# Kernel optimization log

Hardware: AMD Instinct MI355X
Metric: run time of the kernel (lower is better)

The kernel has to match this reference:

```python
import jax, jax.numpy as jnp
import numpy as np

N = 200_000      # total nodes
E = 3_200_000    # directed edges
F = 128          # input features
G = 2_000        # graphs in batch
SIZES = (128, 128, 128, 128, 128, 64)
K = 2            # TAGConv hops
EPS = 1e-5


def setup_inputs() -> dict:
    key = jax.random.key(0)
    ks = jax.random.split(key, 12)
    x = jax.random.normal(ks[0], (N, F), jnp.float32)
    edge_index = jax.random.randint(ks[1], (2, E), 0, N, dtype=jnp.int32).astype(jnp.int64)
    segment_ids = jnp.sort(jax.random.randint(ks[2], (N,), 0, G, dtype=jnp.int32)).astype(jnp.int64)
    conv_W = jax.random.normal(ks[3], (5, (K + 1) * 128, 128), jnp.float32) * 0.05
    conv_W_last = jax.random.normal(ks[4], ((K + 1) * 128, 64), jnp.float32) * 0.05
    bn_gamma = jnp.ones((5, 128), jnp.float32)
    bn_beta = jnp.zeros((5, 128), jnp.float32)
    bn_gamma_last = jnp.ones((64,), jnp.float32)
    bn_beta_last = jnp.zeros((64,), jnp.float32)
    agg_bn_gamma = jnp.ones((4,), jnp.float32)
    agg_bn_beta = jnp.zeros((4,), jnp.float32)
    agg_W = jax.random.normal(ks[5], (64, 4 * 64), jnp.float32) * 0.05
    agg_b = jnp.zeros((64,), jnp.float32)
    out_W = jax.random.normal(ks[6], (1, 64), jnp.float32) * 0.05
    out_b = jnp.zeros((1,), jnp.float32)
    return dict(x=x, edge_index=edge_index, segment_ids=segment_ids, conv_W=conv_W,
                conv_W_last=conv_W_last, bn_gamma=bn_gamma, bn_beta=bn_beta,
                bn_gamma_last=bn_gamma_last, bn_beta_last=bn_beta_last,
                agg_bn_gamma=agg_bn_gamma, agg_bn_beta=agg_bn_beta,
                agg_W=agg_W, agg_b=agg_b, out_W=out_W, out_b=out_b)


def _forward(x, edge_index, segment_ids, conv_W, conv_W_last, bn_gamma, bn_beta,
             bn_gamma_last, bn_beta_last, agg_bn_gamma, agg_bn_beta,
             agg_W, agg_b, out_W, out_b):
    src, dst = edge_index[0], edge_index[1]
    deg = jax.ops.segment_sum(jnp.ones((E,), x.dtype), dst, num_segments=N)
    norm = jnp.where(deg > 0, jax.lax.rsqrt(jnp.maximum(deg, 1.0)), 0.0)[:, None]  # D^{-1/2}

    def prop(h):  # h: [N, d] -> D^{-1/2} A D^{-1/2} h
        return norm * jax.ops.segment_sum((h * norm)[src], dst, num_segments=N)

    def tagconv(h, W):  # concat of A_norm^k h for k=0..K, then linear (no bias; BN follows)
        hs = [h]
        for _ in range(K):
            hs.append(prop(hs[-1]))
        return jnp.concatenate(hs, axis=-1) @ W

    def bn(h, g, b):  # training-mode batchnorm over nodes
        m = h.mean(0)
        v = h.var(0)
        return (h - m) * jax.lax.rsqrt(v + EPS) * g + b

    outs = []
    h = x
    for l in range(len(SIZES)):
        if l < 5:
            W, g, b = conv_W[l], bn_gamma[l], bn_beta[l]
        else:
            W, g, b = conv_W_last, bn_gamma_last, bn_beta_last
        h = jax.nn.relu(bn(tagconv(h, W), g, b))
        if l >= 2 and SIZES[l] == SIZES[l - 2]:  # skip connection
            h = h + outs[l - 2]
        outs.append(h)

    # ragged pooling: (max, min, mean, std) per graph
    counts = jax.ops.segment_sum(jnp.ones((N,), h.dtype), segment_ids, num_segments=G)[:, None]
    s = jax.ops.segment_sum(h, segment_ids, num_segments=G)
    mean = s / jnp.maximum(counts, 1.0)
    ssq = jax.ops.segment_sum(h * h, segment_ids, num_segments=G)
    var = (ssq - counts * mean * mean) / jnp.maximum(counts - 1.0, 1.0)  # unbiased like th.std
    std = jnp.sqrt(jnp.maximum(var, 0.0))
    mx = jax.ops.segment_max(h, segment_ids, num_segments=G)
    mn = jax.ops.segment_min(h, segment_ids, num_segments=G)
    pooled = jnp.stack([mx, mn, mean, std], axis=1)  # [G, 4, 64]

    # aggregation BatchNorm1d over the 4 pooling channels (stats over graphs x feat)
    m = pooled.mean(axis=(0, 2))
    v = pooled.var(axis=(0, 2))
    pooled = (pooled - m[None, :, None]) * jax.lax.rsqrt(v + EPS)[None, :, None] \
             * agg_bn_gamma[None, :, None] + agg_bn_beta[None, :, None]

    flat = pooled.reshape(G, 4 * SIZES[-1])
    hg = flat @ agg_W.T + agg_b           # aggregation Linear(256 -> 64)
    return hg @ out_W.T + out_b           # output Linear(64 -> 1), shape [G, 1]


def reference(x, edge_index, segment_ids, conv_W, conv_W_last, bn_gamma, bn_beta,
              bn_gamma_last, bn_beta_last, agg_bn_gamma, agg_bn_beta,
              agg_W, agg_b, out_W, out_b):
    return _forward(x, edge_index, segment_ids, conv_W, conv_W_last, bn_gamma, bn_beta,
                    bn_gamma_last, bn_beta_last, agg_bn_gamma, agg_bn_beta,
                    agg_W, agg_b, out_W, out_b)
```

## Files before the change

kernel.cpp:

```cpp
#include <hip/hip_runtime.h>
#include <cstddef>
#include <cstdint>

#define N_NODES  200000
#define N_EDGES  3200000
#define N_GRAPHS 2000
#define BN_EPS   1e-5f
#define NB       391
#define BSH      9
#define CHUNK    16384

typedef unsigned int   u32;
typedef unsigned short u16;

using short8   = __attribute__((ext_vector_type(8))) short;
using floatx16 = __attribute__((ext_vector_type(16))) float;

__device__ __forceinline__ float bflo(u32 v) { union {u32 i; float f;} c; c.i = v << 16; return c.f; }
__device__ __forceinline__ float bfhi(u32 v) { union {u32 i; float f;} c; c.i = v & 0xffff0000u; return c.f; }
__device__ __forceinline__ float bf1(u16 v)  { union {u32 i; float f;} c; c.i = ((u32)v) << 16; return c.f; }
__device__ __forceinline__ u32 f2bf(float f) {
    union {float f; u32 i;} c; c.f = f;
    return (c.i + 0x7fffu + ((c.i >> 16) & 1u)) >> 16;
}
__device__ __forceinline__ u32 pack2(float a, float b) { return f2bf(a) | (f2bf(b) << 16); }

__global__ void x2bf_kernel(const float* __restrict__ x, u16* __restrict__ xb, int total4) {
    for (int i = blockIdx.x * 256 + threadIdx.x; i < total4; i += gridDim.x * 256) {
        float4 v = ((const float4*)x)[i];
        uint2 o; o.x = pack2(v.x, v.y); o.y = pack2(v.z, v.w);
        ((uint2*)xb)[i] = o;
    }
}

__global__ void wpack_all(const float* __restrict__ convW, const float* __restrict__ convWlast,
                          u16* __restrict__ whi, u16* __restrict__ wlo) {
    const int PER = 384 * 128;
    int tid = blockIdx.x * 256 + threadIdx.x;
    float w;
    int dst;
    if (tid < 5 * PER) {
        int l = tid / PER, r = tid % PER;
        int k = r / 128, nn = r % 128;
        w = convW[tid];
        dst = l * PER + (k >> 6) * 128 * 64 + nn * 64 + (k & 63);
    } else {
        int r = tid - 5 * PER;
        if (r >= 384 * 64) return;
        int k = r / 64, nn = r % 64;
        w = convWlast[r];
        dst = 5 * PER + (k >> 6) * 64 * 64 + nn * 64 + (k & 63);
    }
    u16 hi = (u16)f2bf(w);
    float rem = w - bf1(hi);
    whi[dst] = hi;
    wlo[dst] = (u16)f2bf(rem);
}

__global__ __launch_bounds__(256)
void bucket_hist(const int* __restrict__ edst, int* __restrict__ bcnt, int e) {
    __shared__ int h[NB];
    for (int t = threadIdx.x; t < NB; t += 256) h[t] = 0;
    __syncthreads();
    int base = blockIdx.x * CHUNK;
    int end  = min(base + CHUNK, e);
    for (int i = base + threadIdx.x; i < end; i += 256)
        atomicAdd(&h[edst[i] >> BSH], 1);
    __syncthreads();
    for (int t = threadIdx.x; t < NB; t += 256)
        if (h[t]) atomicAdd(&bcnt[t], h[t]);
}

__global__ void bucket_scan(const int* __restrict__ bcnt, int* __restrict__ bbase,
                            int* __restrict__ bcur) {
    __shared__ int ls[512];
    int t = threadIdx.x;
    int v = (t < NB) ? bcnt[t] : 0;
    ls[t] = v;
    __syncthreads();
    for (int off = 1; off < 512; off <<= 1) {
        int a = (t >= off) ? ls[t - off] : 0;
        __syncthreads();
        ls[t] += a;
        __syncthreads();
    }
    if (t <= NB) {
        int excl = ls[t] - v;
        bbase[t] = excl;
        if (t < NB) bcur[t] = excl;
    }
}

__global__ __launch_bounds__(256)
void bucket_scatter(const int* __restrict__ esrc, const int* __restrict__ edst,
                    int* __restrict__ bcur, uint2* __restrict__ esorted, int e) {
    __shared__ int h[NB], lbase[NB], lcur[NB];
    for (int t = threadIdx.x; t < NB; t += 256) { h[t] = 0; lcur[t] = 0; }
    __syncthreads();
    int base = blockIdx.x * CHUNK;
    int end  = min(base + CHUNK, e);
    for (int i = base + threadIdx.x; i < end; i += 256)
        atomicAdd(&h[edst[i] >> BSH], 1);
    __syncthreads();
    for (int t = threadIdx.x; t < NB; t += 256)
        lbase[t] = h[t] ? atomicAdd(&bcur[t], h[t]) : 0;
    __syncthreads();
    for (int i = base + threadIdx.x; i < end; i += 256) {
        int d = edst[i];
        int b = d >> BSH;
        int p = lbase[b] + atomicAdd(&lcur[b], 1);
        uint2 ed; ed.x = (u32)esrc[i]; ed.y = (u32)d;
        esorted[p] = ed;
    }
}

__global__ __launch_bounds__(256)
void bucket_fill(const uint2* __restrict__ esorted, const int* __restrict__ bbase,
                 int* __restrict__ rowptr, int* __restrict__ csr,
                 float* __restrict__ normv, int n, int e) {
    __shared__ int cnt[512], loc[512], tsum[256];
    const int b = blockIdx.x;
    const int ebeg = bbase[b], eend = bbase[b + 1];
    const int t = threadIdx.x;
    cnt[t] = 0; cnt[t + 256] = 0;
    __syncthreads();
    for (int i = ebeg + t; i < eend; i += 256)
        atomicAdd(&cnt[esorted[i].y & 511], 1);
    __syncthreads();
    int c0 = cnt[2 * t], c1 = cnt[2 * t + 1];
    tsum[t] = c0 + c1;
    __syncthreads();
    for (int off = 1; off < 256; off <<= 1) {
        int a = (t >= off) ? tsum[t - off] : 0;
        __syncthreads();
        tsum[t] += a;
        __syncthreads();
    }
    int excl = tsum[t] - (c0 + c1);
    loc[2 * t] = excl;
    loc[2 * t + 1] = excl + c0;
    __syncthreads();
    for (int j = t; j < 512; j += 256) {
        int node = (b << 9) + j;
        if (node < n) {
            rowptr[node] = ebeg + loc[j];
            int deg = cnt[j];
            normv[node] = (deg > 0) ? rsqrtf((float)deg) : 0.f;
        }
    }
    if (b == 0 && t == 0) rowptr[n] = e;
    __syncthreads();
    for (int j = t; j < 512; j += 256) cnt[j] = loc[j];
    __syncthreads();
    for (int i = ebeg + t; i < eend; i += 256) {
        uint2 ed = esorted[i];
        int slot = ebeg + atomicAdd(&cnt[ed.y & 511], 1);
        csr[slot] = (int)ed.x;
    }
}

__global__ __launch_bounds__(256)
void prop_kernel(const u16* __restrict__ hin, const float* __restrict__ norm,
                 const int* __restrict__ rowptr, const int* __restrict__ csr,
                 u16* __restrict__ pout, int n) {
    int wave = threadIdx.x >> 6;
    int lane = threadIdx.x & 63;
    int node = blockIdx.x * 4 + wave;
    if (node >= n) return;
    const int q = lane >> 4;
    const int f = (lane & 15) * 8;
    int s = rowptr[node], e = rowptr[node + 1];
    float a0 = 0, a1 = 0, a2 = 0, a3 = 0, a4 = 0, a5 = 0, a6 = 0, a7 = 0;
    int i = s + q;
    if (i + 12 < e) {
        int sn0 = csr[i], sn1 = csr[i + 4], sn2 = csr[i + 8], sn3 = csr[i + 12];
        while (true) {
            float nw0 = norm[sn0], nw1 = norm[sn1], nw2 = norm[sn2], nw3 = norm[sn3];
            uint4 v0 = *(const uint4*)(hin + (size_t)sn0 * 128 + f);
            uint4 v1 = *(const uint4*)(hin + (size_t)sn1 * 128 + f);
            uint4 v2 = *(const uint4*)(hin + (size_t)sn2 * 128 + f);
            uint4 v3 = *(const uint4*)(hin + (size_t)sn3 * 128 + f);
            int ni = i + 16;
            bool more = (ni + 12 < e);
            int t0 = 0, t1 = 0, t2 = 0, t3 = 0;
            if (more) {
                t0 = csr[ni]; t1 = csr[ni + 4]; t2 = csr[ni + 8]; t3 = csr[ni + 12];
            }
            a0 += bflo(v0.x) * nw0 + bflo(v1.x) * nw1 + bflo(v2.x) * nw2 + bflo(v3.x) * nw3;
            a1 += bfhi(v0.x) * nw0 + bfhi(v1.x) * nw1 + bfhi(v2.x) * nw2 + bfhi(v3.x) * nw3;
            a2 += bflo(v0.y) * nw0 + bflo(v1.y) * nw1 + bflo(v2.y) * nw2 + bflo(v3.y) * nw3;
            a3 += bfhi(v0.y) * nw0 + bfhi(v1.y) * nw1 + bfhi(v2.y) * nw2 + bfhi(v3.y) * nw3;
            a4 += bflo(v0.z) * nw0 + bflo(v1.z) * nw1 + bflo(v2.z) * nw2 + bflo(v3.z) * nw3;
            a5 += bfhi(v0.z) * nw0 + bfhi(v1.z) * nw1 + bfhi(v2.z) * nw2 + bfhi(v3.z) * nw3;
            a6 += bflo(v0.w) * nw0 + bflo(v1.w) * nw1 + bflo(v2.w) * nw2 + bflo(v3.w) * nw3;
            a7 += bfhi(v0.w) * nw0 + bfhi(v1.w) * nw1 + bfhi(v2.w) * nw2 + bfhi(v3.w) * nw3;
            i = ni;
            if (!more) break;
            sn0 = t0; sn1 = t1; sn2 = t2; sn3 = t3;
        }
    }
    for (; i < e; i += 4) {
        int sn0 = csr[i];
        float nw0 = norm[sn0];
        uint4 v0 = *(const uint4*)(hin + (size_t)sn0 * 128 + f);
        a0 += bflo(v0.x) * nw0; a1 += bfhi(v0.x) * nw0;
        a2 += bflo(v0.y) * nw0; a3 += bfhi(v0.y) * nw0;
        a4 += bflo(v0.z) * nw0; a5 += bfhi(v0.z) * nw0;
        a6 += bflo(v0.w) * nw0; a7 += bfhi(v0.w) * nw0;
    }
    a0 += __shfl_down(a0, 32, 64); a1 += __shfl_down(a1, 32, 64);
    a2 += __shfl_down(a2, 32, 64); a3 += __shfl_down(a3, 32, 64);
    a4 += __shfl_down(a4, 32, 64); a5 += __shfl_down(a5, 32, 64);
    a6 += __shfl_down(a6, 32, 64); a7 += __shfl_down(a7, 32, 64);
    a0 += __shfl_down(a0, 16, 64); a1 += __shfl_down(a1, 16, 64);
    a2 += __shfl_down(a2, 16, 64); a3 += __shfl_down(a3, 16, 64);
    a4 += __shfl_down(a4, 16, 64); a5 += __shfl_down(a5, 16, 64);
    a6 += __shfl_down(a6, 16, 64); a7 += __shfl_down(a7, 16, 64);
    if (q == 0) {
        float nd = norm[node];
        uint4 o;
        o.x = pack2(a0 * nd, a1 * nd);
        o.y = pack2(a2 * nd, a3 * nd);
        o.z = pack2(a4 * nd, a5 * nd);
        o.w = pack2(a6 * nd, a7 * nd);
        *(uint4*)(pout + (size_t)node * 128 + f) = o;
    }
}

template <int DOUT>
__global__ __launch_bounds__(256)
void gemm_mfma(const u16* __restrict__ A0, const u16* __restrict__ A1,
               const u16* __restrict__ A2, const u16* __restrict__ whi,
               const u16* __restrict__ wlo, u16* __restrict__ outp,
               float* __restrict__ gstats, int n) {
    constexpr int TJ = DOUT / 64;
    constexpr int BELEMS = DOUT * 64;
    __shared__ u16 As[128 * 64];
    __shared__ u16 Bh[BELEMS];
    __shared__ u16 Bl[BELEMS];
    __shared__ float col_s[DOUT];
    __shared__ float col_q[DOUT];

    const int tid  = threadIdx.x;
    const int wave = tid >> 6;
    const int lane = tid & 63;
    const int wrow = wave >> 1;
    const int wcol = wave & 1;
    const int row0 = blockIdx.x * 128;
    const int m    = lane & 31;
    const int half = lane >> 5;

    const u16* mats[3] = {A0, A1, A2};

    floatx16 acc[2][TJ];
#pragma unroll
    for (int ti = 0; ti < 2; ++ti)
#pragma unroll
        for (int tj = 0; tj < TJ; ++tj)
#pragma unroll
            for (int r = 0; r < 16; ++r) acc[ti][tj][r] = 0.f;

    for (int c = 0; c < 6; ++c) {
        const u16* M = mats[c >> 1];
        const int kloc = (c & 1) * 64;
#pragma unroll
        for (int it = 0; it < 4; ++it) {
            int rib  = wave * 32 + it * 8 + (lane >> 3);
            int grow = row0 + rib;
            if (grow >= n) grow = n - 1;
            uint4 v = *(const uint4*)(M + (size_t)grow * 128 + kloc + (lane & 7) * 8);
            int cc = (lane & 7) ^ (rib & 7);
            *(uint4*)&As[rib * 64 + cc * 8] = v;
        }
        {
            const int cbase = c * BELEMS;
#pragma unroll
            for (int j = 0; j < BELEMS / 2048; ++j) {
                int idx  = tid + j * 256;
                int nrow = idx >> 3, seg = idx & 7;
                int dcc  = seg ^ (nrow & 7);
                *(uint4*)&Bh[nrow * 64 + dcc * 8] =
                    *(const uint4*)(whi + cbase + idx * 8);
                *(uint4*)&Bl[nrow * 64 + dcc * 8] =
                    *(const uint4*)(wlo + cbase + idx * 8);
            }
        }
        __syncthreads();
#pragma unroll
        for (int s = 0; s < 4; ++s) {
            const int cc = s * 2 + half;
            short8 a[2], bhf[TJ], blf[TJ];
#pragma unroll
            for (int ti = 0; ti < 2; ++ti) {
                int r = wrow * 64 + ti * 32 + m;
                a[ti] = *(const short8*)&As[r * 64 + ((cc ^ (r & 7)) * 8)];
            }
#pragma unroll
            for (int tj = 0; tj < TJ; ++tj) {
                int rr = wcol * TJ * 32 + tj * 32 + m;
                int off = rr * 64 + ((cc ^ (rr & 7)) * 8);
                bhf[tj] = *(const short8*)&Bh[off];
                blf[tj] = *(const short8*)&Bl[off];
            }
#pragma unroll
            for (int ti = 0; ti < 2; ++ti)
#pragma unroll
                for (int tj = 0; tj < TJ; ++tj) {
                    acc[ti][tj] = __builtin_amdgcn_mfma_f32_32x32x16_bf16(
                        a[ti], bhf[tj], acc[ti][tj], 0, 0, 0);
                    acc[ti][tj] = __builtin_amdgcn_mfma_f32_32x32x16_bf16(
                        a[ti], blf[tj], acc[ti][tj], 0, 0, 0);
                }
        }
        __syncthreads();
    }

    if (tid < DOUT) { col_s[tid] = 0.f; col_q[tid] = 0.f; }
    __syncthreads();
#pragma unroll
    for (int tj = 0; tj < TJ; ++tj) {
        int gcol = (wcol * TJ + tj) * 32 + m;
        float s = 0.f, qq = 0.f;
#pragma unroll
        for (int ti = 0; ti < 2; ++ti)
#pragma unroll
            for (int r = 0; r < 16; ++r) {
                int grow = row0 + wrow * 64 + ti * 32 + (r & 3) + 8 * (r >> 2) + 4 * half;
                if (grow < n) {
                    float v = acc[ti][tj][r];
                    s += v; qq += v * v;
                    outp[(size_t)grow * DOUT + gcol] = (u16)f2bf(v);
                }
            }
        atomicAdd(&col_s[gcol], s);
        atomicAdd(&col_q[gcol], qq);
    }
    __syncthreads();
    if (tid < DOUT) {
        atomicAdd(&gstats[tid], col_s[tid]);
        atomicAdd(&gstats[DOUT + tid], col_q[tid]);
    }
}

template <int DOUT, bool SKIP>
__global__ __launch_bounds__(256)
void bn_apply(u16* __restrict__ h, const float* __restrict__ stats,
              const float* __restrict__ gamma, const float* __restrict__ beta,
              const u16* __restrict__ skip, int total4, float inv_n) {
    constexpr int C4 = DOUT / 4;
    __shared__ float sh_scale[DOUT], sh_shift[DOUT];
    if (threadIdx.x < DOUT) {
        int t = threadIdx.x;
        float mm = stats[t] * inv_n;
        float var = stats[DOUT + t] * inv_n - mm * mm;
        float sc = rsqrtf(var + BN_EPS) * gamma[t];
        sh_scale[t] = sc;
        sh_shift[t] = beta[t] - mm * sc;
    }
    __syncthreads();
    for (int idx = blockIdx.x * 256 + threadIdx.x; idx < total4; idx += gridDim.x * 256) {
        int c4 = (idx % C4) * 4;
        uint2 u = ((const uint2*)h)[idx];
        float v0 = bflo(u.x), v1 = bfhi(u.x), v2 = bflo(u.y), v3 = bfhi(u.y);
        v0 = fmaxf(fmaf(v0, sh_scale[c4 + 0], sh_shift[c4 + 0]), 0.f);
        v1 = fmaxf(fmaf(v1, sh_scale[c4 + 1], sh_shift[c4 + 1]), 0.f);
        v2 = fmaxf(fmaf(v2, sh_scale[c4 + 2], sh_shift[c4 + 2]), 0.f);
        v3 = fmaxf(fmaf(v3, sh_scale[c4 + 3], sh_shift[c4 + 3]), 0.f);
        if (SKIP) {
            uint2 sk = ((const uint2*)skip)[idx];
            v0 += bflo(sk.x); v1 += bfhi(sk.x); v2 += bflo(sk.y); v3 += bfhi(sk.y);
        }
        uint2 o; o.x = pack2(v0, v1); o.y = pack2(v2, v3);
        ((uint2*)h)[idx] = o;
    }
}

__global__ void gstart_kernel(const int* __restrict__ seg, int* __restrict__ gstart,
                              int n, int g_count) {
    int i = blockIdx.x * 256 + threadIdx.x;
    if (i >= n) return;
    int cur = seg[i];
    if (i == 0) {
        for (int g = 0; g <= cur; ++g) gstart[g] = 0;
    } else {
        int prev = seg[i - 1];
        for (int g = prev + 1; g <= cur; ++g) gstart[g] = i;
    }
    if (i == n - 1) {
        for (int g = cur + 1; g <= g_count; ++g) gstart[g] = n;
    }
}

__global__ __launch_bounds__(256)
void pool_kernel(const u16* __restrict__ hraw, const float* __restrict__ stats,
                 const float* __restrict__ gamma, const float* __restrict__ beta,
                 const int* __restrict__ gstart, float* __restrict__ pooled,
                 float* __restrict__ aggstat, int g_count, float inv_n) {
    __shared__ float sagg[8];
    if (threadIdx.x < 8) sagg[threadIdx.x] = 0.f;
    __syncthreads();
    int wave = threadIdx.x >> 6;
    int lane = threadIdx.x & 63;
    int g = blockIdx.x * 4 + wave;
    if (g < g_count) {
        float mmean = stats[lane] * inv_n;
        float var = stats[64 + lane] * inv_n - mmean * mmean;
        float sc = rsqrtf(var + BN_EPS) * gamma[lane];
        float sh = beta[lane] - mmean * sc;
        int s = gstart[g], e = gstart[g + 1];
        float mx = -INFINITY, mn = INFINITY, sm = 0.f, sq = 0.f;
        for (int nidx = s; nidx < e; ++nidx) {
            float v = fmaxf(fmaf(bf1(hraw[(size_t)nidx * 64 + lane]), sc, sh), 0.f);
            mx = fmaxf(mx, v);
            mn = fminf(mn, v);
            sm += v;
            sq += v * v;
        }
        float cnt = (float)(e - s);
        float mean = sm / fmaxf(cnt, 1.f);
        float var2 = (sq - cnt * mean * mean) / fmaxf(cnt - 1.f, 1.f);
        float sd = sqrtf(fmaxf(var2, 0.f));
        size_t base = (size_t)g * 256;
        pooled[base + 0 * 64 + lane] = mx;
        pooled[base + 1 * 64 + lane] = mn;
        pooled[base + 2 * 64 + lane] = mean;
        pooled[base + 3 * 64 + lane] = sd;
        float s0 = mx, s1 = mn, s2 = mean, s3 = sd;
        float q0 = mx * mx, q1 = mn * mn, q2 = mean * mean, q3 = sd * sd;
        for (int off = 32; off > 0; off >>= 1) {
            s0 += __shfl_down(s0, off, 64); q0 += __shfl_down(q0, off, 64);
            s1 += __shfl_down(s1, off, 64); q1 += __shfl_down(q1, off, 64);
            s2 += __shfl_down(s2, off, 64); q2 += __shfl_down(q2, off, 64);
            s3 += __shfl_down(s3, off, 64); q3 += __shfl_down(q3, off, 64);
        }
        if (lane == 0) {
            atomicAdd(&sagg[0], s0); atomicAdd(&sagg[1], q0);
            atomicAdd(&sagg[2], s1); atomicAdd(&sagg[3], q1);
            atomicAdd(&sagg[4], s2); atomicAdd(&sagg[5], q2);
            atomicAdd(&sagg[6], s3); atomicAdd(&sagg[7], q3);
        }
    }
    __syncthreads();
    if (threadIdx.x < 8) atomicAdd(&aggstat[threadIdx.x], sagg[threadIdx.x]);
}

__global__ __launch_bounds__(256)
void final_kernel(const float* __restrict__ pooled, const float* __restrict__ aggstat,
                  const float* __restrict__ agg_gamma, const float* __restrict__ agg_beta,
                  const float* __restrict__ aggW, const float* __restrict__ aggb,
                  const float* __restrict__ outW, const float* __restrict__ outb,
                  float* __restrict__ out, int g_count, float inv_total) {
    __shared__ float sflat[4][256];
    int wave = threadIdx.x >> 6;
    int lane = threadIdx.x & 63;
    int g = blockIdx.x * 4 + wave;
    if (g < g_count) {
#pragma unroll
        for (int c = 0; c < 4; ++c) {
            float v = pooled[(size_t)g * 256 + c * 64 + lane];
            float m = aggstat[c * 2] * inv_total;
            float var = aggstat[c * 2 + 1] * inv_total - m * m;
            v = (v - m) * rsqrtf(var + BN_EPS) * agg_gamma[c] + agg_beta[c];
            sflat[wave][c * 64 + lane] = v;
        }
    }
    __syncthreads();
    if (g < g_count) {
        float acc = aggb[lane];
        const float* wrow = aggW + lane * 256;
#pragma unroll 8
        for (int i = 0; i < 256; ++i)
            acc = fmaf(sflat[wave][i], wrow[i], acc);
        float t = acc * outW[lane];
        for (int off = 32; off > 0; off >>= 1) t += __shfl_down(t, off, 64);
        if (lane == 0) out[g] = t + outb[0];
    }
}

extern "C" void kernel_launch(void* const* d_in, const int* in_sizes, int n_in,
                              void* d_out, int out_size, void* d_ws, size_t ws_size,
                              hipStream_t stream) {
    const int N = N_NODES, E = N_EDGES, G = N_GRAPHS;

    const float* x           = (const float*)d_in[0];
    const int*   ei          = (const int*)d_in[1];
    const int*   seg         = (const int*)d_in[2];
    const float* conv_W      = (const float*)d_in[3];
    const float* conv_W_last = (const float*)d_in[4];
    const float* bn_g        = (const float*)d_in[5];
    const float* bn_b        = (const float*)d_in[6];
    const float* bn_gl       = (const float*)d_in[7];
    const float* bn_bl       = (const float*)d_in[8];
    const float* agg_g       = (const float*)d_in[9];
    const float* agg_bt      = (const float*)d_in[10];
    const float* aggW        = (const float*)d_in[11];
    const float* aggb        = (const float*)d_in[12];
    const float* outW        = (const float*)d_in[13];
    const float* outb        = (const float*)d_in[14];
    float* out = (float*)d_out;

    const int* esrc = ei;
    const int* edst = ei + E;

    size_t off = 0;
    auto alloc = [&](size_t bytes) -> void* {
        void* p = (char*)d_ws + off;
        off += (bytes + 255) & ~(size_t)255;
        return p;
    };
    float* normv  = (float*)alloc((size_t)N * 4);
    int*   rowptr = (int*)alloc((size_t)(N + 1) * 4);
    int*   csr    = (int*)alloc((size_t)E * 4);
    int*   bcnt   = (int*)alloc((NB + 1) * 4);
    int*   bbase  = (int*)alloc((NB + 1) * 4);
    int*   bcur   = (int*)alloc((NB + 1) * 4);
    int*   gstart = (int*)alloc((size_t)(G + 1) * 4);
    float* statsA = (float*)alloc((6 * 256 + 8) * 4);
    float* aggstat= statsA + 6 * 256;
    float* pooled = (float*)alloc((size_t)G * 256 * 4);
    const size_t WPACK = 5 * 384 * 128 + 384 * 64;
    u16*   whip   = (u16*)alloc(WPACK * 2);
    u16*   wlop   = (u16*)alloc(WPACK * 2);
    u16*   ring0  = (u16*)alloc((size_t)N * 128 * 2);
    u16*   ring1  = (u16*)alloc((size_t)N * 128 * 2);
    u16*   ring2  = (u16*)alloc((size_t)N * 128 * 2);
    u16*   p1     = (u16*)alloc((size_t)N * 128 * 2);
    u16*   p2     = (u16*)alloc((size_t)N * 128 * 2);
    u16*   ring[3] = {ring0, ring1, ring2};
    uint2* esorted = (uint2*)p2;

    hipMemsetAsync(bcnt, 0, (NB + 1) * 4, stream);
    hipMemsetAsync(statsA, 0, (6 * 256 + 8) * 4, stream);
    const int nchunk = (E + CHUNK - 1) / CHUNK;
    bucket_hist<<<nchunk, 256, 0, stream>>>(edst, bcnt, E);
    bucket_scan<<<1, 512, 0, stream>>>(bcnt, bbase, bcur);
    bucket_scatter<<<nchunk, 256, 0, stream>>>(esrc, edst, bcur, esorted, E);
    bucket_fill<<<NB, 256, 0, stream>>>(esorted, bbase, rowptr, csr, normv, N, E);

    x2bf_kernel<<<2048, 256, 0, stream>>>(x, ring2, N * 128 / 4);

    wpack_all<<<(5 * 384 * 128 + 384 * 64 + 255) / 256, 256, 0, stream>>>(
        conv_W, conv_W_last, whip, wlop);

    gstart_kernel<<<(N + 255) / 256, 256, 0, stream>>>(seg, gstart, N, G);

    const u16* h_in = ring2;
    const int gemm_grid = (N + 127) / 128;
    const float inv_n = 1.f / (float)N;
    for (int l = 0; l < 6; ++l) {
        const int dout = (l < 5) ? 128 : 64;
        const u16* whi = whip + (size_t)((l < 5) ? l * 384 * 128 : 5 * 384 * 128);
        const u16* wlo = wlop + (size_t)((l < 5) ? l * 384 * 128 : 5 * 384 * 128);
        const float* gamma = (l < 5) ? (bn_g + l * 128) : bn_gl;
        const float* beta  = (l < 5) ? (bn_b + l * 128) : bn_bl;
        float* stats = statsA + l * 256;
        u16* outbuf = ring[l % 3];

        prop_kernel<<<(N + 3) / 4, 256, 0, stream>>>(h_in, normv, rowptr, csr, p1, N);
        prop_kernel<<<(N + 3) / 4, 256, 0, stream>>>(p1, normv, rowptr, csr, p2, N);

        if (dout == 128)
            gemm_mfma<128><<<gemm_grid, 256, 0, stream>>>(h_in, p1, p2, whi, wlo, outbuf,
                                                          stats, N);
        else
            gemm_mfma<64><<<gemm_grid, 256, 0, stream>>>(h_in, p1, p2, whi, wlo, outbuf,
                                                         stats, N);

        if (l < 5) {
            int total4 = N * dout / 4;
            bool has_skip = (l >= 2);
            const u16* skipb = has_skip ? ring[(l - 2) % 3] : nullptr;
            if (has_skip)
                bn_apply<128, true><<<8192, 256, 0, stream>>>(outbuf, stats, gamma, beta,
                                                              skipb, total4, inv_n);
            else
                bn_apply<128, false><<<8192, 256, 0, stream>>>(outbuf, stats, gamma, beta,
                                                               nullptr, total4, inv_n);
        }
        h_in = outbuf;
    }

    pool_kernel<<<(G + 3) / 4, 256, 0, stream>>>(ring[5 % 3], statsA + 5 * 256,
                                                 bn_gl, bn_bl, gstart, pooled, aggstat,
                                                 G, inv_n);
    final_kernel<<<(G + 3) / 4, 256, 0, stream>>>(pooled, aggstat, agg_g, agg_bt,
                                                  aggW, aggb, outW, outb, out, G,
                                                  1.f / (float)(G * 64));
}
```

Baseline: 2.609 ms.

## Reorder last TAGConv layer: project to 64-dim before propagation via Horner scheme

For the final layer (128->64), the input is first multiplied by all three weight blocks (a 192-wide GEMM), and the two sparse propagations then run on 64-wide features in Horner form (A(z2)+z1, then A(u)+z0). This replaces two 128-wide gather passes with two 64-wide ones and shrinks the GEMM's K dimension. BN statistics are gathered by a separate reduction kernel. The cost is a different bf16 rounding order and an extra stats pass over the output.

```diff
diff --git a/kernel.cpp b/kernel.cpp
--- a/kernel.cpp
+++ b/kernel.cpp
@@ -46,10 +46,11 @@
         dst = l * PER + (k >> 6) * 128 * 64 + nn * 64 + (k & 63);
     } else {
         int r = tid - 5 * PER;
-        if (r >= 384 * 64) return;
-        int k = r / 64, nn = r % 64;
-        w = convWlast[r];
-        dst = 5 * PER + (k >> 6) * 64 * 64 + nn * 64 + (k & 63);
+        if (r >= 128 * 192) return;
+        int k = r / 192, n = r % 192;
+        int j = n >> 6, c = n & 63;
+        w = convWlast[(128 * j + k) * 64 + c];
+        dst = 5 * PER + (k >> 6) * 192 * 64 + n * 64 + (k & 63);
     }
     u16 hi = (u16)f2bf(w);
     float rem = w - bf1(hi);
@@ -227,6 +228,86 @@
     }
 }
 
+__global__ __launch_bounds__(256)
+void prop64(const u16* __restrict__ zin, int zstride,
+            const u16* __restrict__ addin, int astride,
+            const float* __restrict__ norm,
+            const int* __restrict__ rowptr, const int* __restrict__ csr,
+            u16* __restrict__ outp, int n) {
+    int wave = threadIdx.x >> 6;
+    int lane = threadIdx.x & 63;
+    int node = blockIdx.x * 4 + wave;
+    if (node >= n) return;
+    const int e8 = lane >> 3;
+    const int f  = (lane & 7) * 8;
+    int s = rowptr[node], e = rowptr[node + 1];
+    float a0 = 0, a1 = 0, a2 = 0, a3 = 0, a4 = 0, a5 = 0, a6 = 0, a7 = 0;
+    int ib = s;
+    if (ib + 16 <= e) {
+        int sn0 = csr[ib + e8], sn1 = csr[ib + 8 + e8];
+        while (true) {
+            float nw0 = norm[sn0], nw1 = norm[sn1];
+            uint4 v0 = *(const uint4*)(zin + (size_t)sn0 * zstride + f);
+            uint4 v1 = *(const uint4*)(zin + (size_t)sn1 * zstride + f);
+            int nb = ib + 16;
+            bool more = (nb + 16 <= e);
+            int t0 = 0, t1 = 0;
+            if (more) { t0 = csr[nb + e8]; t1 = csr[nb + 8 + e8]; }
+            a0 += bflo(v0.x) * nw0 + bflo(v1.x) * nw1;
+            a1 += bfhi(v0.x) * nw0 + bfhi(v1.x) * nw1;
+            a2 += bflo(v0.y) * nw0 + bflo(v1.y) * nw1;
+            a3 += bfhi(v0.y) * nw0 + bfhi(v1.y) * nw1;
+            a4 += bflo(v0.z) * nw0 + bflo(v1.z) * nw1;
+            a5 += bfhi(v0.z) * nw0 + bfhi(v1.z) * nw1;
+            a6 += bflo(v0.w) * nw0 + bflo(v1.w) * nw1;
+            a7 += bfhi(v0.w) * nw0 + bfhi(v1.w) * nw1;
+            ib = nb;
+            if (!more) break;
+            sn0 = t0; sn1 = t1;
+        }
+    }
+    if (ib + e8 < e) {
+        int sn = csr[ib + e8];
+        float nw = norm[sn];
+        uint4 v = *(const uint4*)(zin + (size_t)sn * zstride + f);
+        a0 += bflo(v.x) * nw; a1 += bfhi(v.x) * nw;
+        a2 += bflo(v.y) * nw; a3 += bfhi(v.y) * nw;
+        a4 += bflo(v.z) * nw; a5 += bfhi(v.z) * nw;
+        a6 += bflo(v.w) * nw; a7 += bfhi(v.w) * nw;
+    }
+    if (ib + 8 + e8 < e) {
+        int sn = csr[ib + 8 + e8];
+        float nw = norm[sn];
+        uint4 v = *(const uint4*)(zin + (size_t)sn * zstride + f);
+        a0 += bflo(v.x) * nw; a1 += bfhi(v.x) * nw;
+        a2 += bflo(v.y) * nw; a3 += bfhi(v.y) * nw;
+        a4 += bflo(v.z) * nw; a5 += bfhi(v.z) * nw;
+        a6 += bflo(v.w) * nw; a7 += bfhi(v.w) * nw;
+    }
+    a0 += __shfl_down(a0, 32, 64); a1 += __shfl_down(a1, 32, 64);
+    a2 += __shfl_down(a2, 32, 64); a3 += __shfl_down(a3, 32, 64);
+    a4 += __shfl_down(a4, 32, 64); a5 += __shfl_down(a5, 32, 64);
+    a6 += __shfl_down(a6, 32, 64); a7 += __shfl_down(a7, 32, 64);
+    a0 += __shfl_down(a0, 16, 64); a1 += __shfl_down(a1, 16, 64);
+    a2 += __shfl_down(a2, 16, 64); a3 += __shfl_down(a3, 16, 64);
+    a4 += __shfl_down(a4, 16, 64); a5 += __shfl_down(a5, 16, 64);
+    a6 += __shfl_down(a6, 16, 64); a7 += __shfl_down(a7, 16, 64);
+    a0 += __shfl_down(a0, 8, 64);  a1 += __shfl_down(a1, 8, 64);
+    a2 += __shfl_down(a2, 8, 64);  a3 += __shfl_down(a3, 8, 64);
+    a4 += __shfl_down(a4, 8, 64);  a5 += __shfl_down(a5, 8, 64);
+    a6 += __shfl_down(a6, 8, 64);  a7 += __shfl_down(a7, 8, 64);
+    if (e8 == 0) {
+        float nd = norm[node];
+        uint4 ad = *(const uint4*)(addin + (size_t)node * astride + f);
+        uint4 o;
+        o.x = pack2(bflo(ad.x) + a0 * nd, bfhi(ad.x) + a1 * nd);
+        o.y = pack2(bflo(ad.y) + a2 * nd, bfhi(ad.y) + a3 * nd);
+        o.z = pack2(bflo(ad.z) + a4 * nd, bfhi(ad.z) + a5 * nd);
+        o.w = pack2(bflo(ad.w) + a6 * nd, bfhi(ad.w) + a7 * nd);
+        *(uint4*)(outp + (size_t)node * 64 + f) = o;
+    }
+}
+
 template <int DOUT>
 __global__ __launch_bounds__(256)
 void gemm_mfma(const u16* __restrict__ A0, const u16* __restrict__ A1,
@@ -339,6 +420,118 @@
     if (tid < DOUT) {
         atomicAdd(&gstats[tid], col_s[tid]);
         atomicAdd(&gstats[DOUT + tid], col_q[tid]);
+    }
+}
+
+__global__ __launch_bounds__(256)
+void gemm192(const u16* __restrict__ A, const u16* __restrict__ whi,
+             const u16* __restrict__ wlo, u16* __restrict__ z, int n) {
+    __shared__ u16 As[64 * 64];
+    __shared__ u16 Bh[192 * 64];
+    __shared__ u16 Bl[192 * 64];
+
+    const int tid  = threadIdx.x;
+    const int wave = tid >> 6;
+    const int lane = tid & 63;
+    const int wrow = wave >> 1;
+    const int wcol = wave & 1;
+    const int row0 = blockIdx.x * 64;
+    const int m    = lane & 31;
+    const int half = lane >> 5;
+
+    floatx16 acc[3];
+#pragma unroll
+    for (int tj = 0; tj < 3; ++tj)
+#pragma unroll
+        for (int r = 0; r < 16; ++r) acc[tj][r] = 0.f;
+
+    for (int c = 0; c < 2; ++c) {
+        const int kloc = c * 64;
+#pragma unroll
+        for (int it = 0; it < 2; ++it) {
+            int rib  = it * 32 + (tid >> 3);
+            int grow = row0 + rib;
+            if (grow >= n) grow = n - 1;
+            uint4 v = *(const uint4*)(A + (size_t)grow * 128 + kloc + (tid & 7) * 8);
+            int cc = (tid & 7) ^ (rib & 7);
+            *(uint4*)&As[rib * 64 + cc * 8] = v;
+        }
+        {
+            const int cbase = c * 192 * 64;
+#pragma unroll
+            for (int j = 0; j < 6; ++j) {
+                int idx  = tid + j * 256;
+                int nrow = idx >> 3, seg = idx & 7;
+                int dcc  = seg ^ (nrow & 7);
+                *(uint4*)&Bh[nrow * 64 + dcc * 8] =
+                    *(const uint4*)(whi + cbase + idx * 8);
+                *(uint4*)&Bl[nrow * 64 + dcc * 8] =
+                    *(const uint4*)(wlo + cbase + idx * 8);
+            }
+        }
+        __syncthreads();
+#pragma unroll
+        for (int s = 0; s < 4; ++s) {
+            const int cc = s * 2 + half;
+            short8 a, bhf[3], blf[3];
+            {
+                int r = wrow * 32 + m;
+                a = *(const short8*)&As[r * 64 + ((cc ^ (r & 7)) * 8)];
+            }
+#pragma unroll
+            for (int tj = 0; tj < 3; ++tj) {
+                int rr = wcol * 96 + tj * 32 + m;
+                int off = rr * 64 + ((cc ^ (rr & 7)) * 8);
+                bhf[tj] = *(const short8*)&Bh[off];
+                blf[tj] = *(const short8*)&Bl[off];
+            }
+#pragma unroll
+            for (int tj = 0; tj < 3; ++tj) {
+                acc[tj] = __builtin_amdgcn_mfma_f32_32x32x16_bf16(a, bhf[tj], acc[tj], 0, 0, 0);
+                acc[tj] = __builtin_amdgcn_mfma_f32_32x32x16_bf16(a, blf[tj], acc[tj], 0, 0, 0);
+            }
+        }
+        __syncthreads();
+    }
+#pragma unroll
+    for (int tj = 0; tj < 3; ++tj) {
+        int gcol = wcol * 96 + tj * 32 + m;
+#pragma unroll
+        for (int r = 0; r < 16; ++r) {
+            int grow = row0 + wrow * 32 + (r & 3) + 8 * (r >> 2) + 4 * half;
+            if (grow < n)
+                z[(size_t)grow * 192 + gcol] = (u16)f2bf(acc[tj][r]);
+        }
+    }
+}
+
+__global__ __launch_bounds__(256)
+void bn_stats64(const u16* __restrict__ h, float* __restrict__ stats, int total4) {
+    float s[4] = {0, 0, 0, 0}, q[4] = {0, 0, 0, 0};
+    for (int idx = blockIdx.x * 256 + threadIdx.x; idx < total4; idx += gridDim.x * 256) {
+        uint2 u = ((const uint2*)h)[idx];
+        float v0 = bflo(u.x), v1 = bfhi(u.x), v2 = bflo(u.y), v3 = bfhi(u.y);
+        s[0] += v0; q[0] += v0 * v0;
+        s[1] += v1; q[1] += v1 * v1;
+        s[2] += v2; q[2] += v2 * v2;
+        s[3] += v3; q[3] += v3 * v3;
+    }
+    __shared__ float ls[256][4], lq[256][4];
+#pragma unroll
+    for (int j = 0; j < 4; ++j) { ls[threadIdx.x][j] = s[j]; lq[threadIdx.x][j] = q[j]; }
+    __syncthreads();
+    int t = threadIdx.x;
+    if (t < 16) {
+#pragma unroll 1
+        for (int g = 1; g < 16; ++g) {
+#pragma unroll
+            for (int j = 0; j < 4; ++j) { s[j] += ls[t + g * 16][j]; q[j] += lq[t + g * 16][j]; }
+        }
+#pragma unroll
+        for (int j = 0; j < 4; ++j) {
+            atomicAdd(&stats[t * 4 + j], s[j]);
+            atomicAdd(&stats[64 + t * 4 + j], q[j]);
+        }
     }
 }
 
@@ -518,7 +711,7 @@
     float* statsA = (float*)alloc((6 * 256 + 8) * 4);
     float* aggstat= statsA + 6 * 256;
     float* pooled = (float*)alloc((size_t)G * 256 * 4);
-    const size_t WPACK = 5 * 384 * 128 + 384 * 64;
+    const size_t WPACK = 5 * 384 * 128 + 128 * 192;
     u16*   whip   = (u16*)alloc(WPACK * 2);
     u16*   wlop   = (u16*)alloc(WPACK * 2);
     u16*   ring0  = (u16*)alloc((size_t)N * 128 * 2);
@@ -528,6 +721,7 @@
     u16*   p2     = (u16*)alloc((size_t)N * 128 * 2);
     u16*   ring[3] = {ring0, ring1, ring2};
     uint2* esorted = (uint2*)p2;
+    u16*   zbuf    = p1;
 
     hipMemsetAsync(bcnt, 0, (NB + 1) * 4, stream);
     hipMemsetAsync(statsA, 0, (6 * 256 + 8) * 4, stream);
@@ -539,7 +733,7 @@
 
     x2bf_kernel<<<2048, 256, 0, stream>>>(x, ring2, N * 128 / 4);
 
-    wpack_all<<<(5 * 384 * 128 + 384 * 64 + 255) / 256, 256, 0, stream>>>(
+    wpack_all<<<(5 * 384 * 128 + 128 * 192 + 255) / 256, 256, 0, stream>>>(
         conv_W, conv_W_last, whip, wlop);
 
     gstart_kernel<<<(N + 255) / 256, 256, 0, stream>>>(seg, gstart, N, G);
@@ -547,40 +741,47 @@
     const u16* h_in = ring2;
     const int gemm_grid = (N + 127) / 128;
     const float inv_n = 1.f / (float)N;
-    for (int l = 0; l < 6; ++l) {
-        const int dout = (l < 5) ? 128 : 64;
-        const u16* whi = whip + (size_t)((l < 5) ? l * 384 * 128 : 5 * 384 * 128);
-        const u16* wlo = wlop + (size_t)((l < 5) ? l * 384 * 128 : 5 * 384 * 128);
-        const float* gamma = (l < 5) ? (bn_g + l * 128) : bn_gl;
-        const float* beta  = (l < 5) ? (bn_b + l * 128) : bn_bl;
+    for (int l = 0; l < 5; ++l) {
+        const u16* whi = whip + (size_t)l * 384 * 128;
+        const u16* wlo = wlop + (size_t)l * 384 * 128;
+        const float* gamma = bn_g + l * 128;
+        const float* beta  = bn_b + l * 128;
         float* stats = statsA + l * 256;
         u16* outbuf = ring[l % 3];
 
         prop_kernel<<<(N + 3) / 4, 256, 0, stream>>>(h_in, normv, rowptr, csr, p1, N);
         prop_kernel<<<(N + 3) / 4, 256, 0, stream>>>(p1, normv, rowptr, csr, p2, N);
 
-        if (dout == 128)
-            gemm_mfma<128><<<gemm_grid, 256, 0, stream>>>(h_in, p1, p2, whi, wlo, outbuf,
-                                                          stats, N);
+        gemm_mfma<128><<<gemm_grid, 256, 0, stream>>>(h_in, p1, p2, whi, wlo, outbuf,
+                                                      stats, N);
+
+        int total4 = N * 128 / 4;
+        bool has_skip = (l >= 2);
+        const u16* skipb = has_skip ? ring[(l - 2) % 3] : nullptr;
+        if (has_skip)
+            bn_apply<128, true><<<8192, 256, 0, stream>>>(outbuf, stats, gamma, beta,
+                                                          skipb, total4, inv_n);
         else
-            gemm_mfma<64><<<gemm_grid, 256, 0, stream>>>(h_in, p1, p2, whi, wlo, outbuf,
-                                                         stats, N);
-
-        if (l < 5) {
-            int total4 = N * dout / 4;
-            bool has_skip = (l >= 2);
-            const u16* skipb = has_skip ? ring[(l - 2) % 3] : nullptr;
-            if (has_skip)
-                bn_apply<128, true><<<8192, 256, 0, stream>>>(outbuf, stats, gamma, beta,
-                                                              skipb, total4, inv_n);
-            else
-                bn_apply<128, false><<<8192, 256, 0, stream>>>(outbuf, stats, gamma, beta,
-                                                               nullptr, total4, inv_n);
-        }
+            bn_apply<128, false><<<8192, 256, 0, stream>>>(outbuf, stats, gamma, beta,
+                                                           nullptr, total4, inv_n);
         h_in = outbuf;
     }
 
-    pool_kernel<<<(G + 3) / 4, 256, 0, stream>>>(ring[5 % 3], statsA + 5 * 256,
+    {
+        const u16* whi5 = whip + (size_t)5 * 384 * 128;
+        const u16* wlo5 = wlop + (size_t)5 * 384 * 128;
+        u16* u_buf   = ring0;
+        u16* out_raw = ring2;
+
+        gemm192<<<(N + 63) / 64, 256, 0, stream>>>(h_in, whi5, wlo5, zbuf, N);
+        prop64<<<(N + 3) / 4, 256, 0, stream>>>(zbuf + 128, 192, zbuf + 64, 192,
+                                                normv, rowptr, csr, u_buf, N);
+        prop64<<<(N + 3) / 4, 256, 0, stream>>>(u_buf, 64, zbuf, 192,
+                                                normv, rowptr, csr, out_raw, N);
+        bn_stats64<<<512, 256, 0, stream>>>(out_raw, statsA + 5 * 256, N * 16);
+    }
+
+    pool_kernel<<<(G + 3) / 4, 256, 0, stream>>>(ring2, statsA + 5 * 256,
                                                  bn_gl, bn_bl, gstart, pooled, aggstat,
                                                  G, inv_n);
     final_kernel<<<(G + 3) / 4, 256, 0, stream>>>(pooled, aggstat, agg_g, agg_bt,
```

Result: faster. 2.553 ms (-2.2%).
